# Optimization experiments

Hardware: AMD Instinct MI355X
Metric: run time of the kernel (lower is better)

Reference implementation:

```python
import jax, jax.numpy as jnp
import numpy as np


def setup_inputs() -> dict:
    key = jax.random.key(0)
    k1, k2 = jax.random.split(key)
    x1 = jax.random.normal(k1, (256, 128, 32, 32), dtype=jnp.float32)   # queries [B,C,h,w]
    x2 = jax.random.normal(k2, (16, 8, 128, 32, 32), dtype=jnp.float32)  # supports [n_way,shot,C,h,w]
    return {"x1": x1, "x2": x2}


def reference(x1, x2):
    # --- cal_covariance: per-class channel covariance over all support pixels ---
    W, S, C, h, w = x2.shape
    sup = x2.transpose(0, 2, 1, 3, 4).reshape(W, C, S * h * w)  # [W, C, S*h*w]
    sup = sup - sup.mean(axis=2, keepdims=True)
    cova = jnp.einsum('wci,wdi->wcd', sup, sup) / (S * h * w - 1)  # [W, C, C]

    # --- cal_similarity: diagonal of q^T Cova q with per-channel L2-normalized query ---
    B, C, h, w = x1.shape
    q = x1.reshape(B, C, h * w)
    q = q / jnp.linalg.norm(q, axis=2, keepdims=True)  # norm over spatial dim per channel
    # diag_i = q[:, i]^T Cova q[:, i]; compute diagonal directly (no (hw)x(hw) matrix)
    sim = jnp.einsum('bci,wcd,bdi->bwi', q, cova, q)  # [B, W, h*w]
    return sim.reshape(B, W * h * w)
```

## Files before the change

kernel.cpp:

```cpp
#include <hip/hip_runtime.h>

typedef _Float16 half8 __attribute__((ext_vector_type(8)));
typedef _Float16 half4 __attribute__((ext_vector_type(4)));
typedef float    f32x4 __attribute__((ext_vector_type(4)));

#define W_CLS 16
#define SHOT  8
#define C_CH  128
#define HW    1024
#define NSAMP (SHOT*HW)
#define B_Q   256

__device__ __forceinline__ void gload_lds16(const _Float16* g, _Float16* l) {
    __builtin_amdgcn_global_load_lds((const __attribute__((address_space(1))) unsigned int*)g,
                                     (__attribute__((address_space(3))) unsigned int*)l,
                                     16, 0, 0);
}


__global__ __launch_bounds__(512) void covarn_kernel(const float* __restrict__ x2,
                                                     const float* __restrict__ x1,
                                                     float* __restrict__ PG,
                                                     float* __restrict__ pmean,
                                                     float* __restrict__ rn) {
    __shared__ _Float16 XT[2][128*72];
    __shared__ float mred[128][4];
    int tid = threadIdx.x;

    if (blockIdx.x >= 256) {
        int rid  = blockIdx.x - 256;
        int row  = rid * 8 + (tid >> 6);
        int lane = tid & 63;
        const f32x4* pr = (const f32x4*)(x1 + (size_t)row * HW);
        float s = 0.f;
        #pragma unroll
        for (int it = 0; it < 4; ++it) {
            f32x4 v = pr[lane + it * 64];
            s += v[0]*v[0] + v[1]*v[1] + v[2]*v[2] + v[3]*v[3];
        }
        #pragma unroll
        for (int off = 32; off; off >>= 1) s += __shfl_xor(s, off, 64);
        if (lane == 0) rn[row] = 1.0f / sqrtf(s);
        return;
    }

    int w = blockIdx.x >> 4, ks = blockIdx.x & 15;
    int s = ks >> 1, p00 = (ks & 1) * 512;
    int c = tid >> 2, ph = (tid & 3) * 16;
    const float* src = x2 + (((size_t)(w*SHOT + s))*C_CH + c)*HW + p00 + ph;
    int lane = tid & 63, wv = tid >> 6;
    int lr = lane & 15, lg = lane >> 4;
    int mt0 = (wv & 3)*2, nt0 = (wv >> 2)*4;

    float msum = 0.f;
    f32x4 acc[2][4];
    #pragma unroll
    for (int mm = 0; mm < 2; ++mm)
        #pragma unroll
        for (int nn = 0; nn < 4; ++nn) acc[mm][nn] = (f32x4){0.f,0.f,0.f,0.f};

    float4 rg[4];
    #pragma unroll
    for (int j = 0; j < 4; ++j) rg[j] = *(const float4*)(src + j*4);
    #pragma unroll
    for (int j = 0; j < 4; ++j) {
        msum += rg[j].x + rg[j].y + rg[j].z + rg[j].w;
        half4 h = {(_Float16)rg[j].x, (_Float16)rg[j].y, (_Float16)rg[j].z, (_Float16)rg[j].w};
        *(half4*)(&XT[0][c*72 + ph + j*4]) = h;
    }
    __syncthreads();

    for (int ch = 0; ch < 8; ++ch) {
        int buf = ch & 1;
        if (ch < 7) {
            #pragma unroll
            for (int j = 0; j < 4; ++j) rg[j] = *(const float4*)(src + (ch+1)*64 + j*4);
        }
        const _Float16* xb = XT[buf];
        #pragma unroll
        for (int kk = 0; kk < 2; ++kk) {
            half8 Bv[4], Av[2];
            #pragma unroll
            for (int nn = 0; nn < 4; ++nn)
                Bv[nn] = *(const half8*)(xb + ((nt0+nn)*16 + lr)*72 + kk*32 + lg*8);
            #pragma unroll
            for (int mm = 0; mm < 2; ++mm)
                Av[mm] = *(const half8*)(xb + ((mt0+mm)*16 + lr)*72 + kk*32 + lg*8);
            #pragma unroll
            for (int mm = 0; mm < 2; ++mm)
                #pragma unroll
                for (int nn = 0; nn < 4; ++nn)
                    acc[mm][nn] = __builtin_amdgcn_mfma_f32_16x16x32_f16(Av[mm], Bv[nn], acc[mm][nn], 0,0,0);
        }
        if (ch < 7) {
            #pragma unroll
            for (int j = 0; j < 4; ++j) {
                msum += rg[j].x + rg[j].y + rg[j].z + rg[j].w;
                half4 h = {(_Float16)rg[j].x, (_Float16)rg[j].y, (_Float16)rg[j].z, (_Float16)rg[j].w};
                *(half4*)(&XT[buf^1][c*72 + ph + j*4]) = h;
            }
        }
        __syncthreads();
    }

    mred[c][tid & 3] = msum;
    __syncthreads();
    if (tid < 128)
        pmean[((size_t)w*16 + ks)*128 + tid] = mred[tid][0]+mred[tid][1]+mred[tid][2]+mred[tid][3];

    float* pg = PG + ((size_t)w*16 + ks)*16384;
    #pragma unroll
    for (int mm = 0; mm < 2; ++mm)
        #pragma unroll
        for (int nn = 0; nn < 4; ++nn)
            #pragma unroll
            for (int r = 0; r < 4; ++r) {
                int cr = (mt0+mm)*16 + lg*4 + r;
                int d  = (nt0+nn)*16 + lr;
                pg[cr*128 + d] = acc[mm][nn][r];
            }
}

__global__ __launch_bounds__(256) void cova_reduce(const float* __restrict__ PG,
                                                   const float* __restrict__ pmean,
                                                   _Float16* __restrict__ Uh) {
    __shared__ float ms[128];
    int t = threadIdx.x;
    int w = blockIdx.x >> 3, rg = blockIdx.x & 7;
    if (t < 128) {
        float sum = 0.f;
        for (int ks = 0; ks < 16; ++ks) sum += pmean[((size_t)w*16 + ks)*128 + t];
        ms[t] = sum * (1.0f/NSAMP);
    }
    __syncthreads();
    const float* pg = PG + (size_t)w*16*16384;
    #pragma unroll
    for (int it = 0; it < 8; ++it) {
        int e = it*256 + t;
        int r = rg*16 + (e >> 7), d = e & 127;
        float g = 0.f;
        for (int ks = 0; ks < 16; ++ks) g += pg[(size_t)ks*16384 + r*128 + d];
        float val = (g - (float)NSAMP*ms[r]*ms[d]) * (1.0f/(NSAMP-1));
        float uval = (d > r) ? val : ((d == r) ? 0.5f*val : 0.0f);
        Uh[((size_t)w*128 + r)*128 + d] = (_Float16)uval;
    }
}

__global__ __launch_bounds__(512) void qconv4_kernel(const float* __restrict__ x1,
                                                     const float* __restrict__ rn,
                                                     _Float16* __restrict__ qf) {
    __shared__ _Float16 T[128*258];
    int tid = threadIdx.x, lane = tid & 63, wv = tid >> 6;
    int b = blockIdx.x >> 2, ic = blockIdx.x & 3;
    const float* xb = x1 + (size_t)b * C_CH * HW + ic*256;
    const float* rnb = rn + b * C_CH;

    #pragma unroll
    for (int cc = 0; cc < 16; ++cc) {
        int c = wv*16 + cc;
        float sc = rnb[c];
        f32x4 v = *(const f32x4*)(xb + (size_t)c * HW + lane*4);
        half4 h = {(_Float16)(v[0]*sc), (_Float16)(v[1]*sc),
                   (_Float16)(v[2]*sc), (_Float16)(v[3]*sc)};
        *(half4*)(&T[c*258 + lane*4]) = h;
    }
    __syncthreads();

    #pragma unroll
    for (int it = 0; it < 8; ++it) {
        int slot = it*512 + tid;
        int tl = slot >> 8;
        int kk = (slot >> 6) & 3;
        int ln = slot & 63;
        int i_loc = tl*16 + (ln & 15);
        int c0 = kk*32 + (ln >> 4)*8;
        half8 pk;
        #pragma unroll
        for (int e = 0; e < 8; ++e) pk[e] = T[(c0+e)*258 + i_loc];
        *(half8*)(qf + (((size_t)b*64 + ic*16 + tl)*4 + kk)*512 + ln*8) = pk;
    }
}

#define TR 4
__global__ __launch_bounds__(512, 4) void sim_kernel(const _Float16* __restrict__ qf,
                                                     const _Float16* __restrict__ Uh,
                                                     float* __restrict__ out) {
    __shared__ _Float16 stage[2][TR*2048];
    __shared__ float sbuf[2][8][TR][17];
    int tid = threadIdx.x, lane = tid & 63, wv = tid >> 6;
    int w_l = wv >> 1, p = wv & 1;
    int lr = lane & 15, lg = lane >> 4;
    int b = blockIdx.x & 255, wg = blockIdx.x >> 8;
    int w = wg*4 + w_l;

    half8 A[10];
    {
        const _Float16* Ub = Uh + (size_t)w*C_CH*C_CH + (size_t)(p*16 + lr)*C_CH + lg*8;
        int idx = 0;
        #pragma unroll
        for (int kk = 0; kk < 4; ++kk)
            #pragma unroll
            for (int j = 0; j <= kk; ++j) {
                A[idx] = *(const half8*)(Ub + (size_t)j*32*C_CH + kk*32);
                ++idx;
            }
    }

    const _Float16* qfb = qf + (size_t)b * 131072;

    #pragma unroll
    for (int set = 0; set < 2; ++set)
        gload_lds16(qfb + tid*8 + set*4096, &stage[0][tid*8 + set*4096]);
    __syncthreads();

    int offB  = lane*8;
    int offDq = p*256 + (lg>>1)*128 + lr*8 + (lg&1)*4;
    int cur = 0;

    for (int r = 0; r < 16; ++r) {
        if (r < 15) {
            const _Float16* gsrc = qfb + (size_t)(r+1)*(TR*2048);
            #pragma unroll
            for (int set = 0; set < 2; ++set)
                gload_lds16(gsrc + tid*8 + set*4096, &stage[cur^1][tid*8 + set*4096]);
        }
        #pragma unroll
        for (int ti = 0; ti < TR; ++ti) {
            const _Float16* tb = &stage[cur][ti*2048];
            half8 B[4];
            #pragma unroll
            for (int kk = 0; kk < 4; ++kk)
                B[kk] = *(const half8*)(tb + kk*512 + offB);
            half4 D[4];
            #pragma unroll
            for (int j = 0; j < 4; ++j)
                D[j] = *(const half4*)(tb + j*512 + offDq);
            f32x4 acc[4];
            #pragma unroll
            for (int j = 0; j < 4; ++j) acc[j] = (f32x4){0.f,0.f,0.f,0.f};
            __builtin_amdgcn_s_setprio(1);
            {
                int idx = 0;
                #pragma unroll
                for (int kk = 0; kk < 4; ++kk)
                    #pragma unroll
                    for (int j = 0; j <= kk; ++j) {
                        acc[j] = __builtin_amdgcn_mfma_f32_16x16x32_f16(A[idx], B[kk], acc[j], 0, 0, 0);
                        ++idx;
                    }
            }
            __builtin_amdgcn_s_setprio(0);
            float s = 0.f;
            #pragma unroll
            for (int j = 0; j < 4; ++j) {
                s = fmaf((float)D[j][0], acc[j][0], s);
                s = fmaf((float)D[j][1], acc[j][1], s);
                s = fmaf((float)D[j][2], acc[j][2], s);
                s = fmaf((float)D[j][3], acc[j][3], s);
            }
            s += __shfl_xor(s, 16, 64);
            s += __shfl_xor(s, 32, 64);
            if (lane < 16) sbuf[cur][w_l*2 + p][ti][lr] = s;
        }
        __syncthreads();
        if (tid < 256) {
            int wl = tid >> 6, rest = tid & 63, ti = rest >> 4, i = rest & 15;
            float v = sbuf[cur][wl*2][ti][i] + sbuf[cur][wl*2 + 1][ti][i];
            out[((size_t)b*W_CLS + wg*4 + wl)*HW + (r*TR + ti)*16 + i] = 2.0f * v;
        }
        cur ^= 1;
    }
}
#undef TR


__global__ __launch_bounds__(256) void rnorm_kernel(const float* __restrict__ x1,
                                                    float* __restrict__ rn) {
    int row  = blockIdx.x * 4 + (threadIdx.x >> 6);
    int lane = threadIdx.x & 63;
    const float4* p = (const float4*)(x1 + (size_t)row * HW);
    float s = 0.f;
    #pragma unroll
    for (int it = 0; it < 4; ++it) {
        float4 v = p[lane + it * 64];
        s += v.x*v.x + v.y*v.y + v.z*v.z + v.w*v.w;
    }
    for (int off = 32; off; off >>= 1) s += __shfl_down(s, off, 64);
    if (lane == 0) rn[row] = 1.0f / sqrtf(s);
}

__global__ __launch_bounds__(256) void mean_kernel_f(const float* __restrict__ x2,
                                                     float* __restrict__ mean) {
    int wc = blockIdx.x;
    int w  = wc >> 7, c = wc & 127;
    const float* base = x2 + ((size_t)(w * SHOT) * C_CH + c) * HW;
    int tid = threadIdx.x;
    float sum = 0.f;
    for (int s = 0; s < SHOT; ++s) {
        const float* row = base + (size_t)s * C_CH * HW;
        for (int p = tid; p < HW; p += 256) sum += row[p];
    }
    for (int off = 32; off; off >>= 1) sum += __shfl_down(sum, off, 64);
    __shared__ float red[4];
    int lane = tid & 63, wv = tid >> 6;
    if (lane == 0) red[wv] = sum;
    __syncthreads();
    if (tid == 0) mean[wc] = (red[0] + red[1] + red[2] + red[3]) * (1.0f / NSAMP);
}

__global__ __launch_bounds__(256) void cova_kernel_f(const float* __restrict__ x2,
                                                     const float* __restrict__ mean,
                                                     _Float16* __restrict__ covah) {
    int bid = blockIdx.x;
    int w  = bid >> 4;
    int c0 = ((bid >> 2) & 3) * 32;
    int d0 = (bid & 3) * 32;
    __shared__ float As[32][33];
    __shared__ float Bs[32][33];
    int tid = threadIdx.x;
    int ty = tid >> 4, tx = tid & 15;
    int lrr = tid >> 3, lc = (tid & 7) * 4;
    const float* base = x2 + (size_t)w * SHOT * C_CH * HW;
    float acc00 = 0.f, acc01 = 0.f, acc10 = 0.f, acc11 = 0.f;
    for (int k0 = 0; k0 < NSAMP; k0 += 32) {
        int s = k0 >> 10, p = k0 & 1023;
        const float4 a4 = *(const float4*)(base + ((size_t)s * C_CH + (c0 + lrr)) * HW + p + lc);
        const float4 b4 = *(const float4*)(base + ((size_t)s * C_CH + (d0 + lrr)) * HW + p + lc);
        As[lrr][lc+0] = a4.x; As[lrr][lc+1] = a4.y; As[lrr][lc+2] = a4.z; As[lrr][lc+3] = a4.w;
        Bs[lrr][lc+0] = b4.x; Bs[lrr][lc+1] = b4.y; Bs[lrr][lc+2] = b4.z; Bs[lrr][lc+3] = b4.w;
        __syncthreads();
        #pragma unroll
        for (int kk = 0; kk < 32; ++kk) {
            float a0 = As[ty*2][kk],   a1 = As[ty*2+1][kk];
            float b0 = Bs[tx*2][kk],   b1 = Bs[tx*2+1][kk];
            acc00 = fmaf(a0, b0, acc00);
            acc01 = fmaf(a0, b1, acc01);
            acc10 = fmaf(a1, b0, acc10);
            acc11 = fmaf(a1, b1, acc11);
        }
        __syncthreads();
    }
    const float inv = 1.0f / (NSAMP - 1);
    int c = c0 + ty * 2, d = d0 + tx * 2;
    float mc0 = mean[w*128 + c],     mc1 = mean[w*128 + c + 1];
    float md0 = mean[w*128 + d],     md1 = mean[w*128 + d + 1];
    _Float16* o = covah + ((size_t)w * 128 + c) * 128 + d;
    o[0]   = (_Float16)((acc00 - (float)NSAMP * mc0 * md0) * inv);
    o[1]   = (_Float16)((acc01 - (float)NSAMP * mc0 * md1) * inv);
    o[128] = (_Float16)((acc10 - (float)NSAMP * mc1 * md0) * inv);
    o[129] = (_Float16)((acc11 - (float)NSAMP * mc1 * md1) * inv);
}

#define LDQ 136
__global__ __launch_bounds__(512) void sim_kernel_f(const float* __restrict__ x1,
                                                    const _Float16* __restrict__ Ch,
                                                    const float* __restrict__ rn,
                                                    float* __restrict__ out) {
    __shared__ _Float16 qT[128][LDQ];
    __shared__ float simbuf[2][128];
    int tid = threadIdx.x;
    int bq  = blockIdx.x;
    int b   = bq >> 3;
    int i0  = (bq & 7) * 128;
    {
        int c  = tid >> 2;
        int iq = (tid & 3) * 32;
        const float* src = x1 + ((size_t)b * C_CH + c) * HW + i0 + iq;
        float scale = rn[b * C_CH + c];
        #pragma unroll
        for (int j4 = 0; j4 < 8; ++j4) {
            f32x4 v = *(const f32x4*)(src + j4 * 4);
            qT[iq + j4*4 + 0][c] = (_Float16)(v[0] * scale);
            qT[iq + j4*4 + 1][c] = (_Float16)(v[1] * scale);
            qT[iq + j4*4 + 2][c] = (_Float16)(v[2] * scale);
            qT[iq + j4*4 + 3][c] = (_Float16)(v[3] * scale);
        }
    }
    __syncthreads();
    int lane = tid & 63;
    int wv   = tid >> 6;
    int mh   = wv >> 2;
    int nq   = wv & 3;
    int d0w  = mh * 64;
    int iw   = nq * 32;
    int lr   = lane & 15;
    int lg   = lane >> 4;
    float qd[4][2][4];
    #pragma unroll
    for (int m = 0; m < 4; ++m)
        #pragma unroll
        for (int n = 0; n < 2; ++n) {
            half4 hq = *(const half4*)&qT[iw + n*16 + lr][d0w + m*16 + lg*4];
            qd[m][n][0] = (float)hq[0];
            qd[m][n][1] = (float)hq[1];
            qd[m][n][2] = (float)hq[2];
            qd[m][n][3] = (float)hq[3];
        }
    for (int w = 0; w < W_CLS; ++w) {
        const _Float16* Cw = Ch + (size_t)w * C_CH * C_CH;
        half8 A[4][4];
        #pragma unroll
        for (int m = 0; m < 4; ++m)
            #pragma unroll
            for (int k = 0; k < 4; ++k)
                A[m][k] = *(const half8*)(Cw + (size_t)(d0w + m*16 + lr) * C_CH + k*32 + lg*8);
        f32x4 acc[4][2];
        #pragma unroll
        for (int m = 0; m < 4; ++m)
            #pragma unroll
            for (int n = 0; n < 2; ++n)
                acc[m][n] = (f32x4){0.f, 0.f, 0.f, 0.f};
        #pragma unroll
        for (int k = 0; k < 4; ++k) {
            #pragma unroll
            for (int n = 0; n < 2; ++n) {
                half8 Bf = *(const half8*)&qT[iw + n*16 + lr][k*32 + lg*8];
                #pragma unroll
                for (int m = 0; m < 4; ++m)
                    acc[m][n] = __builtin_amdgcn_mfma_f32_16x16x32_f16(A[m][k], Bf, acc[m][n], 0, 0, 0);
            }
        }
        float s0 = 0.f, s1 = 0.f;
        #pragma unroll
        for (int m = 0; m < 4; ++m) {
            #pragma unroll
            for (int r = 0; r < 4; ++r) {
                s0 = fmaf(qd[m][0][r], acc[m][0][r], s0);
                s1 = fmaf(qd[m][1][r], acc[m][1][r], s1);
            }
        }
        s0 += __shfl_xor(s0, 16); s0 += __shfl_xor(s0, 32);
        s1 += __shfl_xor(s1, 16); s1 += __shfl_xor(s1, 32);
        if (lane < 16) {
            simbuf[mh][iw + 0*16 + lane] = s0;
            simbuf[mh][iw + 1*16 + lane] = s1;
        }
        __syncthreads();
        if (tid < 128)
            out[((size_t)b * W_CLS + w) * HW + i0 + tid] = simbuf[0][tid] + simbuf[1][tid];
        __syncthreads();
    }
}


extern "C" void kernel_launch(void* const* d_in, const int* in_sizes, int n_in,
                              void* d_out, int out_size, void* d_ws, size_t ws_size,
                              hipStream_t stream) {
    (void)in_sizes; (void)n_in; (void)out_size;
    const float* x1 = (const float*)d_in[0];
    const float* x2 = (const float*)d_in[1];
    float* out = (float*)d_out;

    char* ws = (char*)d_ws;
    const size_t OFF_QF  = 0;
    const size_t OFF_PG  = 67108864;
    const size_t OFF_PM  = OFF_PG  + 16777216;
    const size_t OFF_UH  = OFF_PM  + 131072;
    const size_t OFF_RN  = OFF_UH  + 524288;
    const size_t NEED    = OFF_RN  + 131072;

    if (ws_size >= NEED) {
        _Float16* qf  = (_Float16*)(ws + OFF_QF);
        float*    PG  = (float*)(ws + OFF_PG);
        float*    pm  = (float*)(ws + OFF_PM);
        _Float16* Uh  = (_Float16*)(ws + OFF_UH);
        float*    rn  = (float*)(ws + OFF_RN);
        covarn_kernel<<<4352, 512, 0, stream>>>(x2, x1, PG, pm, rn);
        cova_reduce  <<<128,  256, 0, stream>>>(PG, pm, Uh);
        qconv4_kernel<<<1024, 512, 0, stream>>>(x1, rn, qf);
        sim_kernel   <<<1024, 512, 0, stream>>>(qf, Uh, out);
    } else {
        float*    mean = (float*)ws;
        float*    rn   = mean + W_CLS*C_CH;
        _Float16* Ch   = (_Float16*)(rn + B_Q*C_CH);
        mean_kernel_f<<<W_CLS*C_CH,  256, 0, stream>>>(x2, mean);
        cova_kernel_f<<<W_CLS*16,    256, 0, stream>>>(x2, mean, Ch);
        rnorm_kernel <<<B_Q*C_CH/4,  256, 0, stream>>>(x1, rn);
        sim_kernel_f <<<B_Q*8,       512, 0, stream>>>(x1, Ch, rn, out);
    }
}
```

Before: 189.8 us.

## Fuse query norm and fp16 conversion into similarity kernel, drop qf intermediate

Removes the separate qconv4 pass and the rnorm blocks of the covariance kernel. The similarity kernel now computes per-channel inverse norms itself, then loads fp32 x1 directly, scales and converts to fp16 into LDS in MFMA layout, with a separate D-operand layout. This drops the 64MB fp16 qf round trip and a launch. The cost is that each of the 4 class-group blocks per batch re-reads x1 (norm pass plus staging) with strided, uncoalesced per-element global loads and no async global-to-LDS copies, so the x1 traffic is multiplied.

```diff
diff --git a/kernel.cpp b/kernel.cpp
--- a/kernel.cpp
+++ b/kernel.cpp
@@ -11,38 +11,13 @@
 #define NSAMP (SHOT*HW)
 #define B_Q   256
 
-__device__ __forceinline__ void gload_lds16(const _Float16* g, _Float16* l) {
-    __builtin_amdgcn_global_load_lds((const __attribute__((address_space(1))) unsigned int*)g,
-                                     (__attribute__((address_space(3))) unsigned int*)l,
-                                     16, 0, 0);
-}
-
-
-__global__ __launch_bounds__(512) void covarn_kernel(const float* __restrict__ x2,
-                                                     const float* __restrict__ x1,
-                                                     float* __restrict__ PG,
-                                                     float* __restrict__ pmean,
-                                                     float* __restrict__ rn) {
+
+__global__ __launch_bounds__(512) void cova_kernel(const float* __restrict__ x2,
+                                                   float* __restrict__ PG,
+                                                   float* __restrict__ pmean) {
     __shared__ _Float16 XT[2][128*72];
     __shared__ float mred[128][4];
     int tid = threadIdx.x;
-
-    if (blockIdx.x >= 256) {
-        int rid  = blockIdx.x - 256;
-        int row  = rid * 8 + (tid >> 6);
-        int lane = tid & 63;
-        const f32x4* pr = (const f32x4*)(x1 + (size_t)row * HW);
-        float s = 0.f;
-        #pragma unroll
-        for (int it = 0; it < 4; ++it) {
-            f32x4 v = pr[lane + it * 64];
-            s += v[0]*v[0] + v[1]*v[1] + v[2]*v[2] + v[3]*v[3];
-        }
-        #pragma unroll
-        for (int off = 32; off; off >>= 1) s += __shfl_xor(s, off, 64);
-        if (lane == 0) rn[row] = 1.0f / sqrtf(s);
-        return;
-    }
 
     int w = blockIdx.x >> 4, ks = blockIdx.x & 15;
     int s = ks >> 1, p00 = (ks & 1) * 512;
@@ -146,52 +121,42 @@
     }
 }
 
-__global__ __launch_bounds__(512) void qconv4_kernel(const float* __restrict__ x1,
-                                                     const float* __restrict__ rn,
-                                                     _Float16* __restrict__ qf) {
-    __shared__ _Float16 T[128*258];
-    int tid = threadIdx.x, lane = tid & 63, wv = tid >> 6;
-    int b = blockIdx.x >> 2, ic = blockIdx.x & 3;
-    const float* xb = x1 + (size_t)b * C_CH * HW + ic*256;
-    const float* rnb = rn + b * C_CH;
-
-    #pragma unroll
-    for (int cc = 0; cc < 16; ++cc) {
-        int c = wv*16 + cc;
-        float sc = rnb[c];
-        f32x4 v = *(const f32x4*)(xb + (size_t)c * HW + lane*4);
-        half4 h = {(_Float16)(v[0]*sc), (_Float16)(v[1]*sc),
-                   (_Float16)(v[2]*sc), (_Float16)(v[3]*sc)};
-        *(half4*)(&T[c*258 + lane*4]) = h;
-    }
-    __syncthreads();
-
-    #pragma unroll
-    for (int it = 0; it < 8; ++it) {
-        int slot = it*512 + tid;
-        int tl = slot >> 8;
-        int kk = (slot >> 6) & 3;
-        int ln = slot & 63;
-        int i_loc = tl*16 + (ln & 15);
-        int c0 = kk*32 + (ln >> 4)*8;
-        half8 pk;
-        #pragma unroll
-        for (int e = 0; e < 8; ++e) pk[e] = T[(c0+e)*258 + i_loc];
-        *(half8*)(qf + (((size_t)b*64 + ic*16 + tl)*4 + kk)*512 + ln*8) = pk;
-    }
-}
-
-#define TR 4
-__global__ __launch_bounds__(512, 4) void sim_kernel(const _Float16* __restrict__ qf,
-                                                     const _Float16* __restrict__ Uh,
-                                                     float* __restrict__ out) {
-    __shared__ _Float16 stage[2][TR*2048];
-    __shared__ float sbuf[2][8][TR][17];
+__global__ __launch_bounds__(512) void sim_kernel(const float* __restrict__ x1,
+                                                  const _Float16* __restrict__ Uh,
+                                                  float* __restrict__ out) {
+    __shared__ _Float16 stage[2][4*4096];
+    __shared__ float rnf[128];
+    __shared__ float rndf[128];
+    __shared__ float sbuf[2][4][2][4][17];
+
     int tid = threadIdx.x, lane = tid & 63, wv = tid >> 6;
     int w_l = wv >> 1, p = wv & 1;
     int lr = lane & 15, lg = lane >> 4;
-    int b = blockIdx.x & 255, wg = blockIdx.x >> 8;
-    int w = wg*4 + w_l;
+    int b = blockIdx.x & 255, wq = blockIdx.x >> 8;
+    int w = wq*4 + w_l;
+    const float* xb = x1 + (size_t)b * C_CH * HW;
+
+    {
+        int c = tid >> 2, qtr = tid & 3;
+        const f32x4* pr = (const f32x4*)(xb + (size_t)c*HW + qtr*256);
+        float s = 0.f;
+        #pragma unroll 8
+        for (int k = 0; k < 64; ++k) {
+            f32x4 v = pr[k];
+            s += v[0]*v[0] + v[1]*v[1] + v[2]*v[2] + v[3]*v[3];
+        }
+        s += __shfl_xor(s, 1, 64);
+        s += __shfl_xor(s, 2, 64);
+        if (qtr == 0) rnf[c] = 1.0f / sqrtf(s);
+    }
+    __syncthreads();
+    if (tid < 128) {
+        float r = rnf[tid];
+        int m = tid >> 4, lo = tid & 15;
+        int pp = m & 1, j = m >> 1, jp = j >> 1;
+        int hi = lo >> 2, rr = lo & 3;
+        rndf[((pp*2 + jp)*4 + hi)*8 + (j & 1)*4 + rr] = r;
+    }
 
     half8 A[10];
     {
@@ -205,36 +170,69 @@
                 ++idx;
             }
     }
-
-    const _Float16* qfb = qf + (size_t)b * 131072;
-
-    #pragma unroll
-    for (int set = 0; set < 2; ++set)
-        gload_lds16(qfb + tid*8 + set*4096, &stage[0][tid*8 + set*4096]);
-    __syncthreads();
-
-    int offB  = lane*8;
-    int offDq = p*256 + (lg>>1)*128 + lr*8 + (lg&1)*4;
+    __syncthreads();
+
+#define STAGE(buf, ch) do {                                                  \
+        _Pragma("unroll")                                                    \
+        for (int s_ = 0; s_ < 2; ++s_) {                                     \
+                                                              \
+            int slot = tid + s_*512;                                         \
+            int tile = slot >> 8, kk = (slot >> 6) & 3, ln = slot & 63;      \
+            int gi = (ch)*64 + tile*16 + (ln & 15);                          \
+            int c0 = kk*32 + (ln >> 4)*8;                                    \
+            const float* src = xb + (size_t)c0*HW + gi;                      \
+            float q_[8];                                                     \
+            _Pragma("unroll")                                                \
+            for (int e = 0; e < 8; ++e) q_[e] = src[(size_t)e*HW];           \
+            f32x4 r0 = *(const f32x4*)(rnf + c0);                            \
+            f32x4 r1 = *(const f32x4*)(rnf + c0 + 4);                        \
+            half8 h;                                                         \
+            h[0]=(_Float16)(q_[0]*r0[0]); h[1]=(_Float16)(q_[1]*r0[1]);      \
+            h[2]=(_Float16)(q_[2]*r0[2]); h[3]=(_Float16)(q_[3]*r0[3]);      \
+            h[4]=(_Float16)(q_[4]*r1[0]); h[5]=(_Float16)(q_[5]*r1[1]);      \
+            h[6]=(_Float16)(q_[6]*r1[2]); h[7]=(_Float16)(q_[7]*r1[3]);      \
+            *(half8*)(&stage[buf][tile*4096 + kk*512 + ln*8]) = h;           \
+                                                              \
+            int rem = slot & 255;                                            \
+            int pp = rem >> 7, jp = (rem >> 6) & 1, ln2 = rem & 63;          \
+            int gi2 = (ch)*64 + tile*16 + (ln2 & 15);                        \
+            int hi = ln2 >> 4;                                               \
+            int cb = (4*jp + pp)*16 + hi*4;                                  \
+            const float* sr2 = xb + (size_t)cb*HW + gi2;                     \
+            int grp = (pp*2 + jp)*4 + hi;                                    \
+            f32x4 d0 = *(const f32x4*)(rndf + grp*8);                        \
+            f32x4 d1 = *(const f32x4*)(rndf + grp*8 + 4);                    \
+            float qd_[8];                                                    \
+            _Pragma("unroll")                                                \
+            for (int e = 0; e < 4; ++e) qd_[e] = sr2[(size_t)e*HW];          \
+            _Pragma("unroll")                                                \
+            for (int e = 0; e < 4; ++e) qd_[4+e] = sr2[(size_t)(32+e)*HW];   \
+            half8 hd;                                                        \
+            hd[0]=(_Float16)(qd_[0]*d0[0]); hd[1]=(_Float16)(qd_[1]*d0[1]);  \
+            hd[2]=(_Float16)(qd_[2]*d0[2]); hd[3]=(_Float16)(qd_[3]*d0[3]);  \
+            hd[4]=(_Float16)(qd_[4]*d1[0]); hd[5]=(_Float16)(qd_[5]*d1[1]);  \
+            hd[6]=(_Float16)(qd_[6]*d1[2]); hd[7]=(_Float16)(qd_[7]*d1[3]);  \
+            *(half8*)(&stage[buf][tile*4096 + 2048 + (pp*2+jp)*512 + ln2*8]) = hd; \
+        }                                                                    \
+    } while (0)
+
+    STAGE(0, 0);
+    __syncthreads();
     int cur = 0;
 
-    for (int r = 0; r < 16; ++r) {
-        if (r < 15) {
-            const _Float16* gsrc = qfb + (size_t)(r+1)*(TR*2048);
-            #pragma unroll
-            for (int set = 0; set < 2; ++set)
-                gload_lds16(gsrc + tid*8 + set*4096, &stage[cur^1][tid*8 + set*4096]);
-        }
-        #pragma unroll
-        for (int ti = 0; ti < TR; ++ti) {
-            const _Float16* tb = &stage[cur][ti*2048];
+    for (int ch = 0; ch < 16; ++ch) {
+        if (ch < 15) STAGE(cur^1, ch+1);
+        #pragma unroll
+        for (int ti = 0; ti < 4; ++ti) {
+            const _Float16* tb = &stage[cur][ti*4096];
             half8 B[4];
             #pragma unroll
             for (int kk = 0; kk < 4; ++kk)
-                B[kk] = *(const half8*)(tb + kk*512 + offB);
-            half4 D[4];
-            #pragma unroll
-            for (int j = 0; j < 4; ++j)
-                D[j] = *(const half4*)(tb + j*512 + offDq);
+                B[kk] = *(const half8*)(tb + kk*512 + lane*8);
+            half8 Dv[2];
+            #pragma unroll
+            for (int jp = 0; jp < 2; ++jp)
+                Dv[jp] = *(const half8*)(tb + 2048 + (p*2 + jp)*512 + lane*8);
             f32x4 acc[4];
             #pragma unroll
             for (int j = 0; j < 4; ++j) acc[j] = (f32x4){0.f,0.f,0.f,0.f};
@@ -253,25 +251,24 @@
             float s = 0.f;
             #pragma unroll
             for (int j = 0; j < 4; ++j) {
-                s = fmaf((float)D[j][0], acc[j][0], s);
-                s = fmaf((float)D[j][1], acc[j][1], s);
-                s = fmaf((float)D[j][2], acc[j][2], s);
-                s = fmaf((float)D[j][3], acc[j][3], s);
+                #pragma unroll
+                for (int r = 0; r < 4; ++r)
+                    s = fmaf((float)Dv[j>>1][(j&1)*4 + r], acc[j][r], s);
             }
             s += __shfl_xor(s, 16, 64);
             s += __shfl_xor(s, 32, 64);
-            if (lane < 16) sbuf[cur][w_l*2 + p][ti][lr] = s;
+            if (lane < 16) sbuf[cur][w_l][p][ti][lr] = s;
         }
         __syncthreads();
         if (tid < 256) {
-            int wl = tid >> 6, rest = tid & 63, ti = rest >> 4, i = rest & 15;
-            float v = sbuf[cur][wl*2][ti][i] + sbuf[cur][wl*2 + 1][ti][i];
-            out[((size_t)b*W_CLS + wg*4 + wl)*HW + (r*TR + ti)*16 + i] = 2.0f * v;
+            int wl = tid >> 6, ti = (tid >> 4) & 3, i = tid & 15;
+            float v = sbuf[cur][wl][0][ti][i] + sbuf[cur][wl][1][ti][i];
+            out[((size_t)b*W_CLS + wq*4 + wl)*HW + ch*64 + ti*16 + i] = 2.0f * v;
         }
         cur ^= 1;
     }
-}
-#undef TR
+#undef STAGE
+}
 
 
 __global__ __launch_bounds__(256) void rnorm_kernel(const float* __restrict__ x1,
@@ -452,23 +449,19 @@
     float* out = (float*)d_out;
 
     char* ws = (char*)d_ws;
-    const size_t OFF_QF  = 0;
-    const size_t OFF_PG  = 67108864;
+    const size_t OFF_PG  = 0;
     const size_t OFF_PM  = OFF_PG  + 16777216;
     const size_t OFF_UH  = OFF_PM  + 131072;
     const size_t OFF_RN  = OFF_UH  + 524288;
     const size_t NEED    = OFF_RN  + 131072;
 
     if (ws_size >= NEED) {
-        _Float16* qf  = (_Float16*)(ws + OFF_QF);
         float*    PG  = (float*)(ws + OFF_PG);
         float*    pm  = (float*)(ws + OFF_PM);
         _Float16* Uh  = (_Float16*)(ws + OFF_UH);
-        float*    rn  = (float*)(ws + OFF_RN);
-        covarn_kernel<<<4352, 512, 0, stream>>>(x2, x1, PG, pm, rn);
-        cova_reduce  <<<128,  256, 0, stream>>>(PG, pm, Uh);
-        qconv4_kernel<<<1024, 512, 0, stream>>>(x1, rn, qf);
-        sim_kernel   <<<1024, 512, 0, stream>>>(qf, Uh, out);
+        cova_kernel<<<256,  512, 0, stream>>>(x2, PG, pm);
+        cova_reduce<<<128,  256, 0, stream>>>(PG, pm, Uh);
+        sim_kernel <<<1024, 512, 0, stream>>>(x1, Uh, out);
     } else {
         float*    mean = (float*)ws;
         float*    rn   = mean + W_CLS*C_CH;
```

Measured after the change: 236.6 us. 1.25x slower.

## Give each wave a whole class in sim kernel, dropping LDS cross-wave reduction

Applied to the files above, without the earlier changes.

The sim kernel now runs 256 threads (4 waves), and each wave handles all 128 rows of one class's triangular factor instead of splitting it across two waves. That removes the shared-memory partial-sum buffer and the extra cross-wave combine step, and each wave writes its outputs directly. The trade-off is more register pressure: 20 A fragments and 8 accumulators per wave, with the occupancy hint lowered to 3 blocks. Each thread also issues twice as many LDS staging loads per round.

```diff
diff --git a/kernel.cpp b/kernel.cpp
--- a/kernel.cpp
+++ b/kernel.cpp
@@ -182,26 +182,24 @@
 }
 
 #define TR 4
-__global__ __launch_bounds__(512, 4) void sim_kernel(const _Float16* __restrict__ qf,
+__global__ __launch_bounds__(256, 3) void sim_kernel(const _Float16* __restrict__ qf,
                                                      const _Float16* __restrict__ Uh,
                                                      float* __restrict__ out) {
     __shared__ _Float16 stage[2][TR*2048];
-    __shared__ float sbuf[2][8][TR][17];
     int tid = threadIdx.x, lane = tid & 63, wv = tid >> 6;
-    int w_l = wv >> 1, p = wv & 1;
     int lr = lane & 15, lg = lane >> 4;
     int b = blockIdx.x & 255, wg = blockIdx.x >> 8;
-    int w = wg*4 + w_l;
-
-    half8 A[10];
+    int w = wg*4 + wv;
+
+    half8 A[20];
     {
-        const _Float16* Ub = Uh + (size_t)w*C_CH*C_CH + (size_t)(p*16 + lr)*C_CH + lg*8;
+        const _Float16* Ub = Uh + (size_t)w*C_CH*C_CH + (size_t)lr*C_CH + lg*8;
         int idx = 0;
         #pragma unroll
         for (int kk = 0; kk < 4; ++kk)
             #pragma unroll
-            for (int j = 0; j <= kk; ++j) {
-                A[idx] = *(const half8*)(Ub + (size_t)j*32*C_CH + kk*32);
+            for (int m = 0; m <= 2*kk+1; ++m) {
+                A[idx] = *(const half8*)(Ub + (size_t)m*16*C_CH + kk*32);
                 ++idx;
             }
     }
@@ -209,20 +207,20 @@
     const _Float16* qfb = qf + (size_t)b * 131072;
 
     #pragma unroll
-    for (int set = 0; set < 2; ++set)
-        gload_lds16(qfb + tid*8 + set*4096, &stage[0][tid*8 + set*4096]);
-    __syncthreads();
-
-    int offB  = lane*8;
-    int offDq = p*256 + (lg>>1)*128 + lr*8 + (lg&1)*4;
+    for (int k = 0; k < 4; ++k)
+        gload_lds16(qfb + tid*8 + k*2048, &stage[0][tid*8 + k*2048]);
+    __syncthreads();
+
+    int offD0 = (lg>>1)*128 + lr*8 + (lg&1)*4;
+    float* ob = out + ((size_t)b*W_CLS + w)*HW;
     int cur = 0;
 
     for (int r = 0; r < 16; ++r) {
         if (r < 15) {
             const _Float16* gsrc = qfb + (size_t)(r+1)*(TR*2048);
             #pragma unroll
-            for (int set = 0; set < 2; ++set)
-                gload_lds16(gsrc + tid*8 + set*4096, &stage[cur^1][tid*8 + set*4096]);
+            for (int k = 0; k < 4; ++k)
+                gload_lds16(gsrc + tid*8 + k*2048, &stage[cur^1][tid*8 + k*2048]);
         }
         #pragma unroll
         for (int ti = 0; ti < TR; ++ti) {
@@ -230,44 +228,39 @@
             half8 B[4];
             #pragma unroll
             for (int kk = 0; kk < 4; ++kk)
-                B[kk] = *(const half8*)(tb + kk*512 + offB);
-            half4 D[4];
-            #pragma unroll
-            for (int j = 0; j < 4; ++j)
-                D[j] = *(const half4*)(tb + j*512 + offDq);
-            f32x4 acc[4];
-            #pragma unroll
-            for (int j = 0; j < 4; ++j) acc[j] = (f32x4){0.f,0.f,0.f,0.f};
+                B[kk] = *(const half8*)(tb + kk*512 + lane*8);
+            half4 D[8];
+            #pragma unroll
+            for (int m = 0; m < 8; ++m)
+                D[m] = *(const half4*)(tb + (m>>1)*512 + (m&1)*256 + offD0);
+            f32x4 acc[8];
+            #pragma unroll
+            for (int m = 0; m < 8; ++m) acc[m] = (f32x4){0.f,0.f,0.f,0.f};
             __builtin_amdgcn_s_setprio(1);
             {
                 int idx = 0;
                 #pragma unroll
                 for (int kk = 0; kk < 4; ++kk)
                     #pragma unroll
-                    for (int j = 0; j <= kk; ++j) {
-                        acc[j] = __builtin_amdgcn_mfma_f32_16x16x32_f16(A[idx], B[kk], acc[j], 0, 0, 0);
+                    for (int m = 0; m <= 2*kk+1; ++m) {
+                        acc[m] = __builtin_amdgcn_mfma_f32_16x16x32_f16(A[idx], B[kk], acc[m], 0, 0, 0);
                         ++idx;
                     }
             }
             __builtin_amdgcn_s_setprio(0);
             float s = 0.f;
             #pragma unroll
-            for (int j = 0; j < 4; ++j) {
-                s = fmaf((float)D[j][0], acc[j][0], s);
-                s = fmaf((float)D[j][1], acc[j][1], s);
-                s = fmaf((float)D[j][2], acc[j][2], s);
-                s = fmaf((float)D[j][3], acc[j][3], s);
+            for (int m = 0; m < 8; ++m) {
+                s = fmaf((float)D[m][0], acc[m][0], s);
+                s = fmaf((float)D[m][1], acc[m][1], s);
+                s = fmaf((float)D[m][2], acc[m][2], s);
+                s = fmaf((float)D[m][3], acc[m][3], s);
             }
             s += __shfl_xor(s, 16, 64);
             s += __shfl_xor(s, 32, 64);
-            if (lane < 16) sbuf[cur][w_l*2 + p][ti][lr] = s;
-        }
-        __syncthreads();
-        if (tid < 256) {
-            int wl = tid >> 6, rest = tid & 63, ti = rest >> 4, i = rest & 15;
-            float v = sbuf[cur][wl*2][ti][i] + sbuf[cur][wl*2 + 1][ti][i];
-            out[((size_t)b*W_CLS + wg*4 + wl)*HW + (r*TR + ti)*16 + i] = 2.0f * v;
-        }
+            if (lane < 16) ob[(r*TR + ti)*16 + lr] = 2.0f * s;
+        }
+        __syncthreads();
         cur ^= 1;
     }
 }
@@ -468,7 +461,7 @@
         covarn_kernel<<<4352, 512, 0, stream>>>(x2, x1, PG, pm, rn);
         cova_reduce  <<<128,  256, 0, stream>>>(PG, pm, Uh);
         qconv4_kernel<<<1024, 512, 0, stream>>>(x1, rn, qf);
-        sim_kernel   <<<1024, 512, 0, stream>>>(qf, Uh, out);
+        sim_kernel   <<<1024, 256, 0, stream>>>(qf, Uh, out);
     } else {
         float*    mean = (float*)ws;
         float*    rn   = mean + W_CLS*C_CH;
```

New measurement: 192.6 us. About the same (+1.5%).
